# Kernel optimization log

Hardware: AMD Instinct MI355X
Metric: run time of the kernel (lower is better)

Reference implementation:

```python
import jax, jax.numpy as jnp
import numpy as np

EMBED = 256; M = 8; DV = 32; L = 4; K = 4; SCALE = 0.5
LEVELS = [(128, 128), (64, 64), (32, 32), (16, 16)]  # (H_l, W_l), static
S_TOTAL = sum(h * w for h, w in LEVELS)  # 21760


def _linear_params(key, fan_in, fan_out):
    kw, kb = jax.random.split(key)
    lim = 1.0 / np.sqrt(fan_in)
    W = jax.random.uniform(kw, (fan_in, fan_out), minval=-lim, maxval=lim, dtype=jnp.float32)
    b = jax.random.uniform(kb, (fan_out,), minval=-lim, maxval=lim, dtype=jnp.float32)
    return W, b


def setup_inputs() -> dict:
    key = jax.random.key(0)
    ks = jax.random.split(key, 8)
    N, Q = 2, 8192
    W_off, b_off = _linear_params(ks[0], EMBED, M * L * K * 2)
    W_attn, b_attn = _linear_params(ks[1], EMBED, M * L * K)
    W_val, b_val = _linear_params(ks[2], EMBED, M * DV)
    W_out, b_out = _linear_params(ks[3], M * DV, EMBED)
    queries = jax.random.normal(ks[4], (N, Q, EMBED), dtype=jnp.float32)
    query_geometry_logits = jax.random.normal(ks[5], (N, Q, 4), dtype=jnp.float32)
    value = jax.random.normal(ks[6], (N, S_TOTAL, EMBED), dtype=jnp.float32)
    value_mask = jnp.ones((N, S_TOTAL, 1), dtype=jnp.float32)
    return {"queries": queries, "query_geometry_logits": query_geometry_logits,
            "value": value, "value_mask": value_mask,
            "W_off": W_off, "b_off": b_off, "W_attn": W_attn, "b_attn": b_attn,
            "W_val": W_val, "b_val": b_val, "W_out": W_out, "b_out": b_out}


def _bilinear(img_flat, grid, H, W):
    """grid_sample(mode=bilinear, padding=zeros, align_corners=False).
    img_flat: (B, H*W, C); grid: (B, P, 2) with (x, y) in [-1, 1]."""
    x = (grid[..., 0] + 1.0) * (W * 0.5) - 0.5
    y = (grid[..., 1] + 1.0) * (H * 0.5) - 0.5
    x0f, y0f = jnp.floor(x), jnp.floor(y)
    wx, wy = x - x0f, y - y0f
    x0, y0 = x0f.astype(jnp.int32), y0f.astype(jnp.int32)

    def gather(xi, yi, w):
        valid = (xi >= 0) & (xi < W) & (yi >= 0) & (yi < H)
        idx = jnp.clip(yi, 0, H - 1) * W + jnp.clip(xi, 0, W - 1)
        v = jnp.take_along_axis(img_flat, idx[..., None], axis=1)
        return v * (w * valid)[..., None]

    return (gather(x0, y0, (1 - wx) * (1 - wy)) + gather(x0 + 1, y0, wx * (1 - wy))
            + gather(x0, y0 + 1, (1 - wx) * wy) + gather(x0 + 1, y0 + 1, wx * wy))


def _forward(queries, query_geometry_logits, value, value_mask,
             W_off, b_off, W_attn, b_attn, W_val, b_val, W_out, b_out):
    N, Q, _ = queries.shape
    # attention weights: (N, Q, M, L*K), softmax over the L*K sampling points
    attn = jax.nn.softmax((queries @ W_attn + b_attn).reshape(N, Q, M, L * K), axis=-1)
    # sampling offsets: (N, Q, M, L*K, 2)
    deltas = (queries @ W_off + b_off).reshape(N, Q, M, L * K, 2)
    # reference boxes: sigmoid -> (cx, cy, w, h) in [0, 1]
    b_q = jax.nn.sigmoid(query_geometry_logits)
    xy, wh = b_q[..., :2], b_q[..., 2:]
    scale = wh * (1.0 / K) * SCALE                       # (N, Q, 2)
    pos = xy[:, :, None, None, :] + deltas * scale[:, :, None, None, :]  # (N,Q,M,LK,2)
    # value projection + mask
    v_masked = value_mask * (value @ W_val + b_val)      # (N, S, M*DV)
    # collapse (N, M) for per-head grid sampling
    grid = jnp.clip(2.0 * pos.transpose(0, 2, 1, 3, 4).reshape(N * M, Q, L * K, 2) - 1.0, -1.0, 1.0)
    outs, start = [], 0
    for li, (H, W) in enumerate(LEVELS):
        v_l = v_masked[:, start:start + H * W, :].reshape(N, H * W, M, DV)
        v_l = v_l.transpose(0, 2, 1, 3).reshape(N * M, H * W, DV)
        g_l = grid[:, :, K * li:K * (li + 1), :].reshape(N * M, Q * K, 2)
        s_l = _bilinear(v_l, g_l, H, W)                  # (N*M, Q*K, DV)
        outs.append(s_l.reshape(N, M, Q, K, DV))
        start += H * W
    vals = jnp.concatenate(outs, axis=3)                 # (N, M, Q, L*K, DV)
    vals = vals.transpose(0, 2, 1, 3, 4)                 # (N, Q, M, L*K, DV)
    out = jnp.sum(attn[..., None] * vals, axis=3).reshape(N, Q, M * DV)
    return out @ W_out + b_out                           # (N, Q, EMBED)


def reference(queries, query_geometry_logits, value, value_mask,
              W_off, b_off, W_attn, b_attn, W_val, b_val, W_out, b_out):
    return _forward(queries, query_geometry_logits, value, value_mask,
                    W_off, b_off, W_attn, b_attn, W_val, b_val, W_out, b_out)
```

## Files before the change

kernel.cpp:

```cpp
#include <hip/hip_runtime.h>
#include <math.h>

#define EMBED   256
#define M_HEADS 8
#define DVAL    32
#define LK      16
#define S_TOTAL 21760
#define NQ      8192
#define NROWS   (2 * NQ)
#define QBS     16

typedef __attribute__((ext_vector_type(8))) short s16x8;
typedef __attribute__((ext_vector_type(4))) float f32x4;
typedef unsigned short u16;
typedef unsigned int   u32;

__device__ __forceinline__ short f2bf(float f) {
    unsigned u = __float_as_uint(f);
    u += 0x7fffu + ((u >> 16) & 1u);
    return (short)(u >> 16);
}
__device__ __forceinline__ float bf2f(short h) {
    return __uint_as_float(((unsigned)(u16)h) << 16);
}

#define V_OFF     0
#define V_FLTS    5570560
#define PA_OFF    (V_OFF + V_FLTS)
#define PA_FLTS   6291456
#define QHI_OFF   (PA_OFF + PA_FLTS)
#define QPL_FLTS  2097152
#define QLO_OFF   (QHI_OFF + QPL_FLTS)
#define MID_OFF   (QLO_OFF + QPL_FLTS)
#define MID_FLTS  2097152
#define WHI_OFF   (MID_OFF + MID_FLTS)
#define WOA_FLTS  49152
#define WLO_OFF   (WHI_OFF + WOA_FLTS)
#define WV_OFF    (WLO_OFF + WOA_FLTS)
#define WO_OFF    (WV_OFF + 32768)

__global__ __launch_bounds__(256) void prep_kernel(
    const float* __restrict__ q,     u16* __restrict__ qh, u16* __restrict__ ql,
    const float* __restrict__ W_off, const float* __restrict__ W_attn,
    u16* __restrict__ Whi,           u16* __restrict__ Wlo,
    const float* __restrict__ W_val, u16* __restrict__ Wv,
    const float* __restrict__ W_out, u16* __restrict__ Wo)
{
    const int b = blockIdx.x;
    const int t = threadIdx.x;

    if (b < 4096) {
        const int i4 = b * 256 + t;
        const float4 v = ((const float4*)q)[i4];
        short4 h, l;
        h.x = f2bf(v.x); l.x = f2bf(v.x - bf2f(h.x));
        h.y = f2bf(v.y); l.y = f2bf(v.y - bf2f(h.y));
        h.z = f2bf(v.z); l.z = f2bf(v.z - bf2f(h.z));
        h.w = f2bf(v.w); l.w = f2bf(v.w - bf2f(h.w));
        ((short4*)qh)[i4] = h;
        ((short4*)ql)[i4] = l;
    } else if (b < 4096 + 512) {
        const int flat = (b - 4096) * 256 + t;
        const int which = flat >> 16;
        const int e = flat & 65535;
        const int k = e >> 8, c = e & 255;
        const float f = which ? W_out[k * 256 + c] : W_val[k * 256 + c];
        const int kt = k >> 5, qd = (k >> 3) & 3, j = k & 7;
        const int idx = (((kt * 256 + c) << 2) + qd) * 8 + j;
        (which ? Wo : Wv)[idx] = (u16)f2bf(f);
    } else {
        const int flat = (b - 4608) * 256 + t;
        const int k = flat / 384, c = flat - k * 384;
        const float f = (c < 256) ? W_off[k * 256 + c] : W_attn[k * 128 + (c - 256)];
        const short h = f2bf(f);
        const short lo = f2bf(f - bf2f(h));
        const int kt = k >> 5, qd = (k >> 3) & 3, j = k & 7;
        const int idx = (((kt * 384 + c) << 2) + qd) * 8 + j;
        Whi[idx] = (u16)h;
        Wlo[idx] = (u16)lo;
    }
}

__global__ __launch_bounds__(256) void vproj_kernel(
    const float* __restrict__ value,
    const float* __restrict__ vmask,
    const u16* __restrict__ Wpk,
    const float* __restrict__ b_val,
    u16* __restrict__ v_out)
{
    const int t  = threadIdx.x;
    const int w  = t >> 6, l = t & 63;
    const int c  = l & 15, qd = l >> 4;
    const int r0 = blockIdx.y * 128 + w * 32;
    const int c0 = blockIdx.x * 64;

    f32x4 acc[2][4] = {};

    for (int kt = 0; kt < 8; ++kt) {
        s16x8 a[2], b[4];
        #pragma unroll
        for (int mt = 0; mt < 2; ++mt) {
            const float* ap = value + (size_t)(r0 + mt * 16 + c) * EMBED + kt * 32 + qd * 8;
            const float4 a0 = *(const float4*)ap;
            const float4 a1 = *(const float4*)(ap + 4);
            a[mt] = (s16x8){ f2bf(a0.x), f2bf(a0.y), f2bf(a0.z), f2bf(a0.w),
                             f2bf(a1.x), f2bf(a1.y), f2bf(a1.z), f2bf(a1.w) };
        }
        #pragma unroll
        for (int nt = 0; nt < 4; ++nt)
            b[nt] = *(const s16x8*)(Wpk + (((kt * 256 + c0 + nt * 16 + c) << 2) + qd) * 8);
        #pragma unroll
        for (int mt = 0; mt < 2; ++mt)
            #pragma unroll
            for (int nt = 0; nt < 4; ++nt)
                acc[mt][nt] = __builtin_amdgcn_mfma_f32_16x16x32_bf16(a[mt], b[nt], acc[mt][nt], 0, 0, 0);
    }

    #pragma unroll
    for (int mt = 0; mt < 2; ++mt) {
        #pragma unroll
        for (int r = 0; r < 4; ++r) {
            const int grow = r0 + mt * 16 + qd * 4 + r;
            const int n = (grow >= S_TOTAL) ? 1 : 0;
            const int s = grow - n * S_TOTAL;
            const float mk = vmask[grow];
            #pragma unroll
            for (int nt = 0; nt < 4; ++nt) {
                const int col = c0 + nt * 16 + c;
                const int hm = col >> 5, d = col & 31;
                v_out[((size_t)(n * M_HEADS + hm) * S_TOTAL + s) * DVAL + d] =
                    (u16)f2bf((acc[mt][nt][r] + b_val[col]) * mk);
            }
        }
    }
}

__global__ __launch_bounds__(256) void qproj_kernel(
    const u16* __restrict__ q_hi, const u16* __restrict__ q_lo,
    const float* __restrict__ qgl,
    const u16* __restrict__ Whi, const u16* __restrict__ Wlo,
    const float* __restrict__ b_off, const float* __restrict__ b_attn,
    float* __restrict__ pa)
{
    __shared__ float s_off[32][260];
    __shared__ float s_attn[32][132];
    __shared__ float s_geom[32][4];

    const int t  = threadIdx.x;
    const int w  = t >> 6, l = t & 63;
    const int c  = l & 15, qd = l >> 4;
    const int row0 = blockIdx.x * 32;
    const int c0 = w * 96;

    if (t < 32) {
        const float* g = &qgl[(size_t)(row0 + t) * 4];
        s_geom[t][0] = 1.f / (1.f + __expf(-g[0]));
        s_geom[t][1] = 1.f / (1.f + __expf(-g[1]));
        s_geom[t][2] = (1.f / (1.f + __expf(-g[2]))) * 0.125f;
        s_geom[t][3] = (1.f / (1.f + __expf(-g[3]))) * 0.125f;
    }

    f32x4 acc[2][6] = {};

    for (int kt = 0; kt < 8; ++kt) {
        s16x8 ah[2], al[2], bh[6], bl[6];
        #pragma unroll
        for (int mt = 0; mt < 2; ++mt) {
            const size_t ao = (size_t)(row0 + mt * 16 + c) * EMBED + kt * 32 + qd * 8;
            ah[mt] = *(const s16x8*)(q_hi + ao);
            al[mt] = *(const s16x8*)(q_lo + ao);
        }
        #pragma unroll
        for (int nt = 0; nt < 6; ++nt) {
            const int idx = (((kt * 384 + c0 + nt * 16 + c) << 2) + qd) * 8;
            bh[nt] = *(const s16x8*)(Whi + idx);
            bl[nt] = *(const s16x8*)(Wlo + idx);
        }
        #pragma unroll
        for (int mt = 0; mt < 2; ++mt)
            #pragma unroll
            for (int nt = 0; nt < 6; ++nt) {
                acc[mt][nt] = __builtin_amdgcn_mfma_f32_16x16x32_bf16(ah[mt], bh[nt], acc[mt][nt], 0, 0, 0);
                acc[mt][nt] = __builtin_amdgcn_mfma_f32_16x16x32_bf16(ah[mt], bl[nt], acc[mt][nt], 0, 0, 0);
                acc[mt][nt] = __builtin_amdgcn_mfma_f32_16x16x32_bf16(al[mt], bh[nt], acc[mt][nt], 0, 0, 0);
            }
    }

    #pragma unroll
    for (int mt = 0; mt < 2; ++mt)
        #pragma unroll
        for (int nt = 0; nt < 6; ++nt) {
            const int col = c0 + nt * 16 + c;
            #pragma unroll
            for (int r = 0; r < 4; ++r) {
                const int row = mt * 16 + qd * 4 + r;
                if (col < 256) s_off[row][col] = acc[mt][nt][r] + b_off[col];
                else           s_attn[row][col - 256] = acc[mt][nt][r] + b_attn[col - 256];
            }
        }
    __syncthreads();

    {
        const int qi = t >> 3, hm = t & 7;
        float* a = &s_attn[qi][hm * LK];
        float mx = a[0];
        #pragma unroll
        for (int i = 1; i < LK; ++i) mx = fmaxf(mx, a[i]);
        float s = 0.f;
        #pragma unroll
        for (int i = 0; i < LK; ++i) { const float e = __expf(a[i] - mx); a[i] = e; s += e; }
        const float inv = 1.f / s;
        #pragma unroll
        for (int i = 0; i < LK; ++i) a[i] *= inv;
    }
    __syncthreads();

    for (int p = t; p < 32 * 128; p += 256) {
        const int qi = p >> 7;
        const int pt = p & 127;
        const int lvl = (pt & 15) >> 2;
        const float Wl = (float)(128 >> lvl);
        const float px = fmaf(s_off[qi][2 * pt + 0], s_geom[qi][2], s_geom[qi][0]);
        const float py = fmaf(s_off[qi][2 * pt + 1], s_geom[qi][3], s_geom[qi][1]);
        const float gx = fminf(fmaxf(2.f * px - 1.f, -1.f), 1.f);
        const float gy = fminf(fmaxf(2.f * py - 1.f, -1.f), 1.f);
        const float x = (gx + 1.f) * (Wl * 0.5f) - 0.5f;
        const float y = (gy + 1.f) * (Wl * 0.5f) - 0.5f;
        const size_t idx = ((size_t)(row0 + qi) * 128 + pt) * 3;
        pa[idx + 0] = x;
        pa[idx + 1] = y;
        pa[idx + 2] = s_attn[qi][pt];
    }
}

__global__ __launch_bounds__(256) void sample_kernel(
    const float* __restrict__ pa,
    const u16* __restrict__ v_tab,
    u16* __restrict__ mid)
{
    __shared__ int4   s_idx[QBS * 17];
    __shared__ float4 s_w[QBS * 17];

    const int t    = threadIdx.x;
    const int m    = blockIdx.x & 7;
    const int rest = blockIdx.x >> 3;
    const int qc   = rest & 511;
    const int n    = rest >> 9;
    const int q0   = qc * QBS;

    {
        const int qi = t >> 4, lk = t & 15;
        const int lvl   = lk >> 2;
        const int Wl    = 128 >> lvl;
        const int start = (lvl == 0) ? 0 : (lvl == 1) ? 16384 : (lvl == 2) ? 20480 : 21504;

        const size_t prow = ((size_t)(n * NQ + q0 + qi)) * 128 + m * 16 + lk;
        const float x  = pa[prow * 3 + 0];
        const float y  = pa[prow * 3 + 1];
        const float aw = pa[prow * 3 + 2];

        const float x0f = floorf(x), y0f = floorf(y);
        const int   x0 = (int)x0f, y0 = (int)y0f;
        const float wx = x - x0f, wy = y - y0f;

        const float vx0 = (x0 >= 0) ? 1.f : 0.f;
        const float vx1 = (x0 + 1 <= Wl - 1) ? 1.f : 0.f;
        const float vy0 = (y0 >= 0) ? 1.f : 0.f;
        const float vy1 = (y0 + 1 <= Wl - 1) ? 1.f : 0.f;

        const int xc0 = max(x0, 0);
        const int xc1 = min(x0 + 1, Wl - 1);
        const int yc0 = max(y0, 0);
        const int yc1 = min(y0 + 1, Wl - 1);

        const int e = qi * 17 + lk;
        s_idx[e] = make_int4((start + yc0 * Wl + xc0) * DVAL,
                             (start + yc0 * Wl + xc1) * DVAL,
                             (start + yc1 * Wl + xc0) * DVAL,
                             (start + yc1 * Wl + xc1) * DVAL);
        s_w[e] = make_float4(aw * (1.f - wx) * (1.f - wy) * vx0 * vy0,
                             aw * wx * (1.f - wy) * vx1 * vy0,
                             aw * (1.f - wx) * wy * vx0 * vy1,
                             aw * wx * wy * vx1 * vy1);
    }
    __syncthreads();

    const int g = t >> 4, dp = t & 15;
    const u16* __restrict__ vbp =
        v_tab + (size_t)(n * M_HEADS + m) * S_TOTAL * DVAL + 2 * dp;

    float acc0 = 0.f, acc1 = 0.f;
    #pragma unroll
    for (int lk = 0; lk < LK; ++lk) {
        const int4   id = s_idx[g * 17 + lk];
        const float4 w  = s_w[g * 17 + lk];
        const u32 u0 = *(const u32*)(vbp + id.x);
        const u32 u1 = *(const u32*)(vbp + id.y);
        const u32 u2 = *(const u32*)(vbp + id.z);
        const u32 u3 = *(const u32*)(vbp + id.w);
        acc0 = fmaf(w.x, __uint_as_float(u0 << 16), acc0);
        acc1 = fmaf(w.x, __uint_as_float(u0 & 0xffff0000u), acc1);
        acc0 = fmaf(w.y, __uint_as_float(u1 << 16), acc0);
        acc1 = fmaf(w.y, __uint_as_float(u1 & 0xffff0000u), acc1);
        acc0 = fmaf(w.z, __uint_as_float(u2 << 16), acc0);
        acc1 = fmaf(w.z, __uint_as_float(u2 & 0xffff0000u), acc1);
        acc0 = fmaf(w.w, __uint_as_float(u3 << 16), acc0);
        acc1 = fmaf(w.w, __uint_as_float(u3 & 0xffff0000u), acc1);
    }

    const u32 packed = ((u32)(u16)f2bf(acc1) << 16) | (u32)(u16)f2bf(acc0);
    *(u32*)(mid + ((size_t)(n * NQ + q0 + g)) * EMBED + m * DVAL + 2 * dp) = packed;
}

__global__ __launch_bounds__(256) void out_kernel(
    const u16* __restrict__ mid,
    const u16* __restrict__ Wpk,
    const float* __restrict__ b_out,
    float* __restrict__ out)
{
    const int t  = threadIdx.x;
    const int w  = t >> 6, l = t & 63;
    const int c  = l & 15, qd = l >> 4;
    const int r0 = blockIdx.y * 128 + w * 32;
    const int c0 = blockIdx.x * 64;

    f32x4 acc[2][4] = {};

    for (int kt = 0; kt < 8; ++kt) {
        s16x8 a[2], b[4];
        #pragma unroll
        for (int mt = 0; mt < 2; ++mt)
            a[mt] = *(const s16x8*)(mid + (size_t)(r0 + mt * 16 + c) * EMBED + kt * 32 + qd * 8);
        #pragma unroll
        for (int nt = 0; nt < 4; ++nt)
            b[nt] = *(const s16x8*)(Wpk + (((kt * 256 + c0 + nt * 16 + c) << 2) + qd) * 8);
        #pragma unroll
        for (int mt = 0; mt < 2; ++mt)
            #pragma unroll
            for (int nt = 0; nt < 4; ++nt)
                acc[mt][nt] = __builtin_amdgcn_mfma_f32_16x16x32_bf16(a[mt], b[nt], acc[mt][nt], 0, 0, 0);
    }

    #pragma unroll
    for (int mt = 0; mt < 2; ++mt)
        #pragma unroll
        for (int r = 0; r < 4; ++r) {
            const int row = r0 + mt * 16 + qd * 4 + r;
            #pragma unroll
            for (int nt = 0; nt < 4; ++nt) {
                const int col = c0 + nt * 16 + c;
                out[(size_t)row * EMBED + col] = acc[mt][nt][r] + b_out[col];
            }
        }
}

extern "C" void kernel_launch(void* const* d_in, const int* in_sizes, int n_in,
                              void* d_out, int out_size, void* d_ws, size_t ws_size,
                              hipStream_t stream) {
    (void)in_sizes; (void)n_in; (void)out_size; (void)ws_size;

    const float* queries = (const float*)d_in[0];
    const float* qgl     = (const float*)d_in[1];
    const float* value   = (const float*)d_in[2];
    const float* vmask   = (const float*)d_in[3];
    const float* W_off   = (const float*)d_in[4];
    const float* b_off   = (const float*)d_in[5];
    const float* W_attn  = (const float*)d_in[6];
    const float* b_attn  = (const float*)d_in[7];
    const float* W_val   = (const float*)d_in[8];
    const float* b_val   = (const float*)d_in[9];
    const float* W_out   = (const float*)d_in[10];
    const float* b_out   = (const float*)d_in[11];

    float* ws   = (float*)d_ws;
    u16*  v_ws  = (u16*)(ws + V_OFF);
    float* pa   = ws + PA_OFF;
    u16*  q_hi  = (u16*)(ws + QHI_OFF);
    u16*  q_lo  = (u16*)(ws + QLO_OFF);
    u16*  mid   = (u16*)(ws + MID_OFF);
    u16*  whi   = (u16*)(ws + WHI_OFF);
    u16*  wlo   = (u16*)(ws + WLO_OFF);
    u16*  wvpk  = (u16*)(ws + WV_OFF);
    u16*  wopk  = (u16*)(ws + WO_OFF);
    float* outp = (float*)d_out;

    prep_kernel<<<4992, 256, 0, stream>>>(queries, q_hi, q_lo,
                                          W_off, W_attn, whi, wlo,
                                          W_val, wvpk, W_out, wopk);

    vproj_kernel<<<dim3(4, 340), 256, 0, stream>>>(value, vmask, wvpk, b_val, v_ws);
    qproj_kernel<<<NROWS / 32, 256, 0, stream>>>(q_hi, q_lo, qgl, whi, wlo,
                                                 b_off, b_attn, pa);
    sample_kernel<<<2 * (NQ / QBS) * M_HEADS, 256, 0, stream>>>(pa, v_ws, mid);
    out_kernel<<<dim3(4, 128), 256, 0, stream>>>(mid, wopk, b_out, outp);
}
```

Before: 221.0 us.

## Retile value projection so each wave computes all 256 output columns

The value projection kernel now gives each wave 16 rows and all 256 output columns, instead of 32 rows by 64 columns across a 4-wide column grid. Each fp32 value row is therefore read from global memory and converted to bf16 once, not four times. The cost is that the packed weights are reloaded per wave, and 16 accumulators plus 16 B fragments per lane raise register pressure, which may lower occupancy.

```diff
diff --git a/kernel.cpp b/kernel.cpp
--- a/kernel.cpp
+++ b/kernel.cpp
@@ -91,46 +91,37 @@
     const int t  = threadIdx.x;
     const int w  = t >> 6, l = t & 63;
     const int c  = l & 15, qd = l >> 4;
-    const int r0 = blockIdx.y * 128 + w * 32;
-    const int c0 = blockIdx.x * 64;
-
-    f32x4 acc[2][4] = {};
+    const int r0 = blockIdx.x * 64 + w * 16;
+
+    f32x4 acc[16] = {};
 
     for (int kt = 0; kt < 8; ++kt) {
-        s16x8 a[2], b[4];
-        #pragma unroll
-        for (int mt = 0; mt < 2; ++mt) {
-            const float* ap = value + (size_t)(r0 + mt * 16 + c) * EMBED + kt * 32 + qd * 8;
-            const float4 a0 = *(const float4*)ap;
-            const float4 a1 = *(const float4*)(ap + 4);
-            a[mt] = (s16x8){ f2bf(a0.x), f2bf(a0.y), f2bf(a0.z), f2bf(a0.w),
-                             f2bf(a1.x), f2bf(a1.y), f2bf(a1.z), f2bf(a1.w) };
-        }
-        #pragma unroll
-        for (int nt = 0; nt < 4; ++nt)
-            b[nt] = *(const s16x8*)(Wpk + (((kt * 256 + c0 + nt * 16 + c) << 2) + qd) * 8);
-        #pragma unroll
-        for (int mt = 0; mt < 2; ++mt)
-            #pragma unroll
-            for (int nt = 0; nt < 4; ++nt)
-                acc[mt][nt] = __builtin_amdgcn_mfma_f32_16x16x32_bf16(a[mt], b[nt], acc[mt][nt], 0, 0, 0);
+        const float* ap = value + (size_t)(r0 + c) * EMBED + kt * 32 + qd * 8;
+        const float4 a0 = *(const float4*)ap;
+        const float4 a1 = *(const float4*)(ap + 4);
+        const s16x8 a = (s16x8){ f2bf(a0.x), f2bf(a0.y), f2bf(a0.z), f2bf(a0.w),
+                                 f2bf(a1.x), f2bf(a1.y), f2bf(a1.z), f2bf(a1.w) };
+        s16x8 b[16];
+        #pragma unroll
+        for (int nt = 0; nt < 16; ++nt)
+            b[nt] = *(const s16x8*)(Wpk + (((kt * 256 + nt * 16 + c) << 2) + qd) * 8);
+        #pragma unroll
+        for (int nt = 0; nt < 16; ++nt)
+            acc[nt] = __builtin_amdgcn_mfma_f32_16x16x32_bf16(a, b[nt], acc[nt], 0, 0, 0);
     }
 
     #pragma unroll
-    for (int mt = 0; mt < 2; ++mt) {
-        #pragma unroll
-        for (int r = 0; r < 4; ++r) {
-            const int grow = r0 + mt * 16 + qd * 4 + r;
-            const int n = (grow >= S_TOTAL) ? 1 : 0;
-            const int s = grow - n * S_TOTAL;
-            const float mk = vmask[grow];
-            #pragma unroll
-            for (int nt = 0; nt < 4; ++nt) {
-                const int col = c0 + nt * 16 + c;
-                const int hm = col >> 5, d = col & 31;
-                v_out[((size_t)(n * M_HEADS + hm) * S_TOTAL + s) * DVAL + d] =
-                    (u16)f2bf((acc[mt][nt][r] + b_val[col]) * mk);
-            }
+    for (int r = 0; r < 4; ++r) {
+        const int grow = r0 + qd * 4 + r;
+        const int n = (grow >= S_TOTAL) ? 1 : 0;
+        const int s = grow - n * S_TOTAL;
+        const float mk = vmask[grow];
+        #pragma unroll
+        for (int nt = 0; nt < 16; ++nt) {
+            const int col = nt * 16 + c;
+            const int hm = col >> 5, d = col & 31;
+            v_out[((size_t)(n * M_HEADS + hm) * S_TOTAL + s) * DVAL + d] =
+                (u16)f2bf((acc[nt][r] + b_val[col]) * mk);
         }
     }
 }
@@ -388,7 +379,7 @@
                                           W_off, W_attn, whi, wlo,
                                           W_val, wvpk, W_out, wopk);
 
-    vproj_kernel<<<dim3(4, 340), 256, 0, stream>>>(value, vmask, wvpk, b_val, v_ws);
+    vproj_kernel<<<680, 256, 0, stream>>>(value, vmask, wvpk, b_val, v_ws);
     qproj_kernel<<<NROWS / 32, 256, 0, stream>>>(q_hi, q_lo, qgl, whi, wlo,
                                                  b_off, b_attn, pa);
     sample_kernel<<<2 * (NQ / QBS) * M_HEADS, 256, 0, stream>>>(pa, v_ws, mid);
```

Result: no change. 223.2 us (+1.0%).
